# Kernel optimization log

Measured on AMD Instinct MI355X. Metric: run time of the kernel, lower is better.

## Reference

```python
import jax, jax.numpy as jnp
import numpy as np

PATCH_SIZE = 24
ALPHA = 0.2  # LeakyReLU negative slope


def setup_inputs() -> dict:
    key = jax.random.key(0)
    k_x, k_adj, k_w, k_wc = jax.random.split(key, 4)
    B, T, N, Cin, Cout = 2, 96, 64, 16, 32
    x = jax.random.normal(k_x, (B, T, N, Cin), dtype=jnp.float32)
    adj = jax.random.uniform(k_adj, (N, N), dtype=jnp.float32)  # weighted adjacency in [0,1)
    # xavier_uniform with gain=1.414 on (Cin, Cout)
    limit = 1.414 * float(np.sqrt(6.0 / (Cin + Cout)))
    W = jax.random.uniform(k_w, (Cin, Cout), dtype=jnp.float32, minval=-limit, maxval=limit)
    W_c = jax.random.uniform(k_wc, (Cout,), dtype=jnp.float32, minval=-0.1, maxval=0.1)
    return {"x": x, "adj": adj, "W": W, "W_c": W_c}


def reference(x, adj, W, W_c):
    B, T, N, Cin = x.shape
    P = PATCH_SIZE
    NP = T // P
    Cout = W.shape[1]
    # torch.view semantics == row-major jnp.reshape (faithful, even though it mixes axes)
    x_patched = x.reshape(B, NP, N, P, Cin)
    h = x_patched @ W  # (B, NP, N, P, Cout)
    # vectorized over patches: per-patch outer product over nodes
    e = jnp.einsum('bsipc,bsjpc->bsijpc', h, h)  # (B, NP, N, N, P, Cout)
    e = jnp.where(e >= 0, e, ALPHA * e)  # LeakyReLU
    e = e * adj[None, None, :, :, None, None]
    e = jax.nn.softmax(e, axis=-1)  # softmax over channel dim (as in original)
    # torch.stack(list, dim=4) of (b,i,j,p,c) over patch index -> (B,N,N,P,NP,C)
    e = jnp.transpose(e, (0, 2, 3, 4, 1, 5))
    attention = e.reshape(B, N, N, T, Cout)  # (B, N, N, T, Cout)
    # h_patched.permute(0,2,1,3,4).reshape(B,N,T,C)
    h_flat = jnp.transpose(h, (0, 2, 1, 3, 4)).reshape(B, N, T, Cout)
    # einsum('bnqtc,bntc->bntc') == sum over q then elementwise multiply
    h_prime = attention.sum(axis=2) * h_flat
    return attention, jax.nn.elu(h_prime)
```

## Files before the change

### kernel.cpp

```cpp
#include <hip/hip_runtime.h>
#include <math.h>

#define Bq 2
#define Tq 96
#define Nq 64
#define CIN 16
#define COUT 32
#define PATCH 24
#define NPq 4
#define ATT_SIZE (Bq * Nq * Nq * Tq * COUT)
#define H_ROWS (Bq * NPq * Nq * PATCH)

typedef float f4 __attribute__((ext_vector_type(4)));

__global__ __launch_bounds__(256) void h_gemm_kernel(
    const float* __restrict__ x, const float* __restrict__ W,
    float* __restrict__ h) {
    __shared__ float Wl[CIN * COUT];
    __shared__ float xs[8 * CIN];
    int tid = threadIdx.x;
    Wl[tid]       = W[tid];
    Wl[tid + 256] = W[tid + 256];
    if (tid < 8 * CIN) xs[tid] = x[blockIdx.x * (8 * CIN) + tid];
    __syncthreads();
    int rl = tid >> 5;
    int c  = tid & 31;
    float acc = 0.f;
#pragma unroll
    for (int k = 0; k < CIN; ++k)
        acc += xs[rl * CIN + k] * Wl[k * COUT + c];
    h[blockIdx.x * 256 + tid] = acc;
}

__global__ __launch_bounds__(768) void att_fused_kernel(
    const float* __restrict__ h, const float* __restrict__ adj,
    float* __restrict__ att, float* __restrict__ hprime) {
    const int bi = blockIdx.x;
    const int s  = bi & 3;
    const int i  = (bi >> 2) & 63;
    const int b  = bi >> 8;
    const int tid  = threadIdx.x;
    const int c0   = (tid & 7) * 4;
    const int p    = (tid >> 3) % PATCH;
    const int jsub = tid / 192;
    const int j0   = jsub * 16;

    __shared__ float adjrow[Nq];
    __shared__ f4 red[768];
    if (tid < Nq) adjrow[tid] = adj[i * Nq + tid];
    __syncthreads();

    const float* hb = h + (size_t)((b * NPq + s) * Nq) * (PATCH * COUT);
    const f4 hi = *(const f4*)(hb + (i * PATCH + p) * COUT + c0);

    f4 acc = {0.f, 0.f, 0.f, 0.f};
    const int t = p * NPq + s;
    size_t outbase = ((size_t)((b * Nq + i) * Nq + j0) * Tq + t) * COUT + c0;
    const size_t jstride = (size_t)Tq * COUT;

#pragma unroll 4
    for (int jj = 0; jj < 16; ++jj) {
        const f4 hj = *(const f4*)(hb + ((j0 + jj) * PATCH + p) * COUT + c0);
        const float aj = adjrow[j0 + jj];

        f4 e = hi * hj;
        e.x = fmaxf(e.x, 0.2f * e.x) * aj;
        e.y = fmaxf(e.y, 0.2f * e.y) * aj;
        e.z = fmaxf(e.z, 0.2f * e.z) * aj;
        e.w = fmaxf(e.w, 0.2f * e.w) * aj;

        f4 ex;
        ex.x = __expf(e.x); ex.y = __expf(e.y);
        ex.z = __expf(e.z); ex.w = __expf(e.w);
        float sm = (ex.x + ex.y) + (ex.z + ex.w);
#pragma unroll
        for (int d = 1; d < 8; d <<= 1) sm += __shfl_xor(sm, d);
        const float inv = __builtin_amdgcn_rcpf(sm);
        f4 a = ex * inv;
        acc += a;
        __builtin_nontemporal_store(a, (f4*)(att + outbase + (size_t)jj * jstride));
    }

    red[tid] = acc;
    __syncthreads();

    if (jsub == 0) {
        const f4 a0 = red[tid];
        const f4 a1 = red[tid + 192];
        const f4 a2 = red[tid + 384];
        const f4 a3 = red[tid + 576];
        f4 asum = (a0 + a1) + (a2 + a3);

        const int s2 = t / PATCH;
        const int p2 = t % PATCH;
        const f4 hv = *(const f4*)(h + (size_t)((b * NPq + s2) * Nq + i) * (PATCH * COUT)
                                     + p2 * COUT + c0);
        f4 v = asum * hv;
        v.x = v.x >= 0.f ? v.x : expm1f(v.x);
        v.y = v.y >= 0.f ? v.y : expm1f(v.y);
        v.z = v.z >= 0.f ? v.z : expm1f(v.z);
        v.w = v.w >= 0.f ? v.w : expm1f(v.w);
        *(f4*)(hprime + ((size_t)((b * Nq + i) * Tq + t)) * COUT + c0) = v;
    }
}

extern "C" void kernel_launch(void* const* d_in, const int* in_sizes, int n_in,
                              void* d_out, int out_size, void* d_ws, size_t ws_size,
                              hipStream_t stream) {
    (void)in_sizes; (void)n_in; (void)out_size; (void)ws_size;
    const float* x   = (const float*)d_in[0];
    const float* adj = (const float*)d_in[1];
    const float* W   = (const float*)d_in[2];

    float* h   = (float*)d_ws;
    float* att = (float*)d_out;
    float* hp  = (float*)d_out + ATT_SIZE;

    hipLaunchKernelGGL(h_gemm_kernel, dim3(H_ROWS / 8), dim3(256), 0, stream,
                       x, W, h);
    hipLaunchKernelGGL(att_fused_kernel, dim3(Bq * Nq * NPq), dim3(768), 0, stream,
                       h, adj, att, hp);
}
```

Before: 31.41 us.

## Split j range across blocks so each block writes contiguous t rows

Each attention block now covers one quarter of the j nodes for all 96 time steps, instead of one patch for all j. Every j iteration therefore writes a contiguous 12 KB run of the attention output rather than strided chunks. The per-block shared-memory reduction is replaced by partial sums written to workspace, and a third kernel sums them and applies ELU. This adds a kernel launch and extra global traffic for the partial sums.

```diff
diff --git a/kernel.cpp b/kernel.cpp
--- a/kernel.cpp
+++ b/kernel.cpp
@@ -8,8 +8,12 @@
 #define COUT 32
 #define PATCH 24
 #define NPq 4
+#define JC 4
+#define JPER (Nq / JC)
 #define ATT_SIZE (Bq * Nq * Nq * Tq * COUT)
+#define HP_SIZE (Bq * Nq * Tq * COUT)
 #define H_ROWS (Bq * NPq * Nq * PATCH)
+#define SLAB (Nq * PATCH * COUT)
 
 typedef float f4 __attribute__((ext_vector_type(4)));
 
@@ -32,36 +36,35 @@
     h[blockIdx.x * 256 + tid] = acc;
 }
 
-__global__ __launch_bounds__(768) void att_fused_kernel(
+__global__ __launch_bounds__(768) void att_kernel(
     const float* __restrict__ h, const float* __restrict__ adj,
-    float* __restrict__ att, float* __restrict__ hprime) {
+    float* __restrict__ att, float* __restrict__ part) {
     const int bi = blockIdx.x;
-    const int s  = bi & 3;
+    const int jc = bi & 3;
     const int i  = (bi >> 2) & 63;
     const int b  = bi >> 8;
-    const int tid  = threadIdx.x;
-    const int c0   = (tid & 7) * 4;
-    const int p    = (tid >> 3) % PATCH;
-    const int jsub = tid / 192;
-    const int j0   = jsub * 16;
+    const int j0 = jc * JPER;
+    const int tid = threadIdx.x;
+    const int c0 = (tid & 7) * 4;
+    const int t  = tid >> 3;
+    const int s  = t & 3;
+    const int p  = t >> 2;
 
-    __shared__ float adjrow[Nq];
-    __shared__ f4 red[768];
-    if (tid < Nq) adjrow[tid] = adj[i * Nq + tid];
+    __shared__ float adjrow[JPER];
+    if (tid < JPER) adjrow[tid] = adj[i * Nq + j0 + tid];
     __syncthreads();
 
-    const float* hb = h + (size_t)((b * NPq + s) * Nq) * (PATCH * COUT);
-    const f4 hi = *(const f4*)(hb + (i * PATCH + p) * COUT + c0);
+    const float* hslab = h + (size_t)(b * NPq + s) * SLAB;
+    const f4 hi = *(const f4*)(hslab + (i * PATCH + p) * COUT + c0);
 
     f4 acc = {0.f, 0.f, 0.f, 0.f};
-    const int t = p * NPq + s;
     size_t outbase = ((size_t)((b * Nq + i) * Nq + j0) * Tq + t) * COUT + c0;
     const size_t jstride = (size_t)Tq * COUT;
 
 #pragma unroll 4
-    for (int jj = 0; jj < 16; ++jj) {
-        const f4 hj = *(const f4*)(hb + ((j0 + jj) * PATCH + p) * COUT + c0);
-        const float aj = adjrow[j0 + jj];
+    for (int jj = 0; jj < JPER; ++jj) {
+        const f4 hj = *(const f4*)(hslab + ((j0 + jj) * PATCH + p) * COUT + c0);
+        const float aj = adjrow[jj];
 
         f4 e = hi * hj;
         e.x = fmaxf(e.x, 0.2f * e.x) * aj;
@@ -81,27 +84,38 @@
         __builtin_nontemporal_store(a, (f4*)(att + outbase + (size_t)jj * jstride));
     }
 
-    red[tid] = acc;
-    __syncthreads();
+    float* pp = part + (size_t)jc * HP_SIZE
+                     + ((size_t)((b * Nq + i) * Tq + t)) * COUT + c0;
+    *(f4*)pp = acc;
+}
 
-    if (jsub == 0) {
-        const f4 a0 = red[tid];
-        const f4 a1 = red[tid + 192];
-        const f4 a2 = red[tid + 384];
-        const f4 a3 = red[tid + 576];
-        f4 asum = (a0 + a1) + (a2 + a3);
+__global__ __launch_bounds__(256) void hprime_kernel(
+    const float* __restrict__ part, const float* __restrict__ h,
+    float* __restrict__ hprime) {
+    const int vid  = blockIdx.x * 256 + threadIdx.x;
+    const int base = vid * 4;
+    const int c  = base & 31;
+    const int t  = (base >> 5) % Tq;
+    const int bi = base / (COUT * Tq);
+    const int i  = bi & 63;
+    const int b  = bi >> 6;
 
-        const int s2 = t / PATCH;
-        const int p2 = t % PATCH;
-        const f4 hv = *(const f4*)(h + (size_t)((b * NPq + s2) * Nq + i) * (PATCH * COUT)
-                                     + p2 * COUT + c0);
-        f4 v = asum * hv;
-        v.x = v.x >= 0.f ? v.x : expm1f(v.x);
-        v.y = v.y >= 0.f ? v.y : expm1f(v.y);
-        v.z = v.z >= 0.f ? v.z : expm1f(v.z);
-        v.w = v.w >= 0.f ? v.w : expm1f(v.w);
-        *(f4*)(hprime + ((size_t)((b * Nq + i) * Tq + t)) * COUT + c0) = v;
-    }
+    f4 a0 = *(const f4*)(part + base);
+    f4 a1 = *(const f4*)(part + base + HP_SIZE);
+    f4 a2 = *(const f4*)(part + base + 2 * HP_SIZE);
+    f4 a3 = *(const f4*)(part + base + 3 * HP_SIZE);
+    f4 asum = (a0 + a1) + (a2 + a3);
+
+    const int s2 = t / PATCH;
+    const int p2 = t % PATCH;
+    const f4 hv = *(const f4*)(h + (size_t)((b * NPq + s2) * Nq + i) * (PATCH * COUT)
+                                 + p2 * COUT + c);
+    f4 v = asum * hv;
+    v.x = v.x >= 0.f ? v.x : expm1f(v.x);
+    v.y = v.y >= 0.f ? v.y : expm1f(v.y);
+    v.z = v.z >= 0.f ? v.z : expm1f(v.z);
+    v.w = v.w >= 0.f ? v.w : expm1f(v.w);
+    *(f4*)(hprime + base) = v;
 }
 
 extern "C" void kernel_launch(void* const* d_in, const int* in_sizes, int n_in,
@@ -112,12 +126,15 @@
     const float* adj = (const float*)d_in[1];
     const float* W   = (const float*)d_in[2];
 
-    float* h   = (float*)d_ws;
-    float* att = (float*)d_out;
-    float* hp  = (float*)d_out + ATT_SIZE;
+    float* h    = (float*)d_ws;
+    float* part = (float*)d_ws + H_ROWS * COUT;
+    float* att  = (float*)d_out;
+    float* hp   = (float*)d_out + ATT_SIZE;
 
     hipLaunchKernelGGL(h_gemm_kernel, dim3(H_ROWS / 8), dim3(256), 0, stream,
                        x, W, h);
-    hipLaunchKernelGGL(att_fused_kernel, dim3(Bq * Nq * NPq), dim3(768), 0, stream,
-                       h, adj, att, hp);
+    hipLaunchKernelGGL(att_kernel, dim3(Bq * Nq * JC), dim3(768), 0, stream,
+                       h, adj, att, part);
+    hipLaunchKernelGGL(hprime_kernel, dim3(HP_SIZE / 4 / 256), dim3(256), 0, stream,
+                       part, h, hp);
 }
```

After: 35.08 us. 11.7% more time.
